# Kernel optimization log

Hardware: AMD Instinct MI355X
Metric: run time of the kernel (lower is better)

The kernel has to match this reference:

```python
import jax, jax.numpy as jnp
import numpy as np

DIM = 1024
N_HEADS = 16
HEAD_DIM = DIM // N_HEADS
MAX_SEQ_LEN = 2048
B, T = 2, 2048


def build_rope_cache(max_seq_len, head_dim):
    half_dim = head_dim // 2
    freq_seq = jnp.arange(half_dim, dtype=jnp.float32)
    inv_freq = 1.0 / 10000.0 ** (freq_seq / half_dim)
    t = jnp.arange(max_seq_len, dtype=jnp.float32)
    freqs = jnp.outer(t, inv_freq)                      # [S, half]
    emb = jnp.concatenate((freqs, freqs), axis=-1)      # [S, head_dim]
    cos = jnp.cos(emb)[None, :, None, :]                # [1, S, 1, head_dim]
    sin = jnp.sin(emb)[None, :, None, :]
    return cos, sin


def apply_rope(x, cos, sin):
    # x: [B, T, H, Dh]; cos/sin: [1, T, 1, Dh]
    x_even = x[..., ::2]
    x_odd = x[..., 1::2]
    cos_even = cos[..., ::2]
    sin_even = sin[..., ::2]
    x_even_rot = x_even * cos_even - x_odd * sin_even
    x_odd_rot = x_even * sin_even + x_odd * cos_even
    x_rot = jnp.stack([x_even_rot, x_odd_rot], axis=-1)  # [B,T,H,Dh/2,2]
    return x_rot.reshape(x.shape)


def setup_inputs() -> dict:
    key = jax.random.key(0)
    k1, k2, k3, k4, k5 = jax.random.split(key, 5)
    s = 0.02
    return {
        "x": jax.random.normal(k1, (B, T, DIM), dtype=jnp.float32),
        "attention_mask": jnp.ones((B, T), dtype=bool),
        "qkv_w": jax.random.normal(k2, (3 * DIM, DIM), dtype=jnp.float32) * s,
        "qkv_b": jax.random.normal(k3, (3 * DIM,), dtype=jnp.float32) * s,
        "out_w": jax.random.normal(k4, (DIM, DIM), dtype=jnp.float32) * s,
        "out_b": jax.random.normal(k5, (DIM,), dtype=jnp.float32) * s,
    }


def reference(x, attention_mask, qkv_w, qkv_b, out_w, out_b):
    Bx, Tx, _ = x.shape
    H, Dh = N_HEADS, HEAD_DIM
    scale = Dh ** (-0.5)

    qkv = x @ qkv_w.T + qkv_b                            # [B,T,3*dim]
    qkv = qkv.reshape(Bx, Tx, 3, H, Dh)
    q, k, v = qkv[:, :, 0], qkv[:, :, 1], qkv[:, :, 2]   # [B,T,H,Dh]

    cos, sin = build_rope_cache(MAX_SEQ_LEN, Dh)
    cos_all = cos[:, :Tx]
    sin_all = sin[:, :Tx]
    k = apply_rope(k, cos_all, sin_all)
    q = apply_rope(q, cos_all, sin_all)  # past_len = 0

    scores = jnp.einsum("bthd,bshd->bhts", q, k) * scale  # [B,H,T,S]

    causal = jnp.arange(Tx)[None, :] <= jnp.arange(Tx)[:, None]  # [T,S]
    scores = jnp.where(causal[None, None, :, :], scores, -jnp.inf)
    pad = attention_mask[:, None, None, :]                        # [B,1,1,S]
    scores = jnp.where(pad, scores, -jnp.inf)

    probs = jax.nn.softmax(scores, axis=-1)
    out = jnp.einsum("bhts,bshd->bthd", probs, v)        # [B,T,H,Dh]
    out = out.reshape(Bx, Tx, H * Dh)
    out = out @ out_w.T + out_b
    return out
```

## Files before the change

kernel.cpp:

```cpp
#include <hip/hip_runtime.h>
#include <stdint.h>

#define B_    2
#define T_    2048
#define DIM_  1024
#define NH_   16
#define DH_   64
#define MTOK  (B_*T_)

typedef __attribute__((ext_vector_type(8))) short bf16x8;
typedef __attribute__((ext_vector_type(4))) float f32x4;
typedef __attribute__((ext_vector_type(4))) short short4v;

__device__ __forceinline__ short f2bf(float f){
  union { float f; uint32_t u; } v; v.f = f;
  uint32_t u = v.u;
  return (short)((u + 0x7fffu + ((u>>16)&1u)) >> 16);
}

#define GLDS(g, l) __builtin_amdgcn_global_load_lds( \
    (const __attribute__((address_space(1))) void*)(g), \
    (__attribute__((address_space(3))) void*)(l), 16, 0, 0)

__global__ void convert_all(const float* __restrict__ x, const float* __restrict__ wq,
                            const float* __restrict__ wo,
                            short* __restrict__ xb, short* __restrict__ wqb,
                            short* __restrict__ wob, float* __restrict__ tbl){
  const int NX = MTOK*DIM_/4;
  const int NW = 3*DIM_*DIM_/4;
  const int NO = DIM_*DIM_/4;
  const int total = NX + NW + NO;
  const int gtid = blockIdx.x*blockDim.x + threadIdx.x;
  if (gtid < T_*32){
    int t = gtid >> 5, j = gtid & 31;
    float f = powf(10000.f, -(float)((2*j) & 31) / 32.f);
    float ang = (float)t * f;
    tbl[gtid*2]   = cosf(ang);
    tbl[gtid*2+1] = sinf(ang);
  }
  for (int i = gtid; i < total; i += gridDim.x*blockDim.x){
    const float* src; short* dst; int j;
    if (i < NX){ src = x;  dst = xb;  j = i; }
    else if (i < NX+NW){ src = wq; dst = wqb; j = i-NX; }
    else { src = wo; dst = wob; j = i-NX-NW; }
    float4 v = ((const float4*)src)[j];
    short4v o;
    o.x = f2bf(v.x); o.y = f2bf(v.y); o.z = f2bf(v.z); o.w = f2bf(v.w);
    ((short4v*)dst)[j] = o;
  }
}

template<int MODE>
__global__ __launch_bounds__(256,2)
void gemm_bt(const short* __restrict__ A, const short* __restrict__ Bw,
             const float* __restrict__ bias, float* __restrict__ outf,
             short* __restrict__ qb, short* __restrict__ kb, short* __restrict__ vb,
             const float* __restrict__ rtbl, int K, int N)
{
  __shared__ char smem[65536];
  const int tid  = threadIdx.x;
  const int wave = tid >> 6, lane = tid & 63;
  const int gx = gridDim.x;
  const int nwg = gx * gridDim.y;
  const int lid = blockIdx.x + blockIdx.y * gx;
  const int cpx = nwg >> 3;
  const int swz = (lid & 7) * cpx + (lid >> 3);
  const int bm = (swz / gx) << 7, bn = (swz % gx) << 7;
  const int wm = (wave >> 1) << 6, wn = (wave & 1) << 6;
  const int r16 = lane & 15, g4 = lane >> 4;
  const int slr = lane >> 3, slc = (lane & 7) << 4;

  f32x4 acc[4][4] = {};
  const int nt = K >> 6;

  auto stage = [&](int t, int buf){
    char* As = smem + (buf<<15);
    char* Bs = As + 16384;
    const int k0 = t << 6;
    #pragma unroll
    for (int sg = 0; sg < 4; ++sg){
      int row = (wave<<5) + (sg<<3) + slr;
      GLDS((const char*)A  + ((size_t)(bm+row)*K + k0)*2 + (slc ^ ((row&7)<<4)),
           As + ((wave<<5)+(sg<<3))*128);
      GLDS((const char*)Bw + ((size_t)(bn+row)*K + k0)*2 + (slc ^ ((row&7)<<4)),
           Bs + ((wave<<5)+(sg<<3))*128);
    }
  };

  stage(0, 0);
  asm volatile("s_waitcnt vmcnt(0)" ::: "memory");
  __syncthreads();

  for (int t = 0; t < nt; ++t){
    const int cur = t & 1;
    if (t + 1 < nt) stage(t+1, cur^1);
    char* As = smem + (cur<<15);
    char* Bs = As + 16384;
    #pragma unroll
    for (int ks = 0; ks < 2; ++ks){
      bf16x8 af[4], bfr[4];
      int bo = (ks<<6) + (g4<<4);
      #pragma unroll
      for (int mf = 0; mf < 4; ++mf){
        int row = wm + (mf<<4) + r16;
        af[mf] = *(const bf16x8*)(As + row*128 + (bo ^ ((row&7)<<4)));
      }
      #pragma unroll
      for (int nf = 0; nf < 4; ++nf){
        int row = wn + (nf<<4) + r16;
        bfr[nf] = *(const bf16x8*)(Bs + row*128 + (bo ^ ((row&7)<<4)));
      }
      __builtin_amdgcn_s_setprio(1);
      #pragma unroll
      for (int mf = 0; mf < 4; ++mf)
        #pragma unroll
        for (int nf = 0; nf < 4; ++nf)
          acc[mf][nf] = __builtin_amdgcn_mfma_f32_16x16x32_bf16(af[mf], bfr[nf], acc[mf][nf], 0, 0, 0);
      __builtin_amdgcn_s_setprio(0);
    }
    asm volatile("s_waitcnt vmcnt(0)" ::: "memory");
    __syncthreads();
  }

  if (MODE == 0){
    #pragma unroll
    for (int nf = 0; nf < 4; ++nf){
      int gn = bn + wn + (nf<<4) + r16;
      float bv = bias[gn];
      #pragma unroll
      for (int mf = 0; mf < 4; ++mf)
        #pragma unroll
        for (int j = 0; j < 4; ++j){
          int gm = bm + wm + (mf<<4) + (g4<<2) + j;
          outf[(size_t)gm*N + gn] = acc[mf][nf][j] + bv;
        }
    }
  } else {
    const int s = bn >> 10;
    if (s < 2){
      short* dst = s ? kb : qb;
      const float scq = s ? 1.0f : 0.125f;
      #pragma unroll
      for (int nf = 0; nf < 4; ++nf){
        int gn = bn + wn + (nf<<4) + r16;
        int d = gn & 63, h = (gn >> 6) & 15;
        int u = d >> 1;
        float sgn = (d & 1) ? 1.f : -1.f;
        float bv = bias[gn];
        #pragma unroll
        for (int mf = 0; mf < 4; ++mf){
          #pragma unroll
          for (int j = 0; j < 4; ++j){
            int gm = bm + wm + (mf<<4) + (g4<<2) + j;
            int b = gm >> 11, t = gm & (T_-1);
            float val = acc[mf][nf][j] + bv;
            float prt = __shfl_xor(val, 1);
            float2 cssn = ((const float2*)rtbl)[(t<<5) + u];
            float out = (val*cssn.x + prt*sgn*cssn.y) * scq;
            dst[(((size_t)(b*NH_+h))*T_ + t)*DH_ + d] = f2bf(out);
          }
        }
      }
    } else {
      #pragma unroll
      for (int nf = 0; nf < 4; ++nf){
        int gn = bn + wn + (nf<<4) + r16;
        int d = gn & 63, h = (gn >> 6) & 15;
        float bv = bias[gn];
        #pragma unroll
        for (int mf = 0; mf < 4; ++mf){
          int gm0 = bm + wm + (mf<<4) + (g4<<2);
          int b = gm0 >> 11, t0 = gm0 & (T_-1);
          short* vrow = vb + ((size_t)((b*NH_+h)*DH_ + d))*T_ + (t0 & ~63);
          int lo = t0 & 15, hi = (t0 & 63) >> 4;
          #pragma unroll
          for (int j = 0; j < 4; ++j)
            vrow[((lo + j) << 2) + hi] = f2bf(acc[mf][nf][j] + bv);
        }
      }
    }
  }
}

__global__ __launch_bounds__(256,2)
void attn_fwd(const short* __restrict__ q, const short* __restrict__ k,
              const short* __restrict__ vt, short* __restrict__ o)
{
  __shared__ char smem[40960];
  const int lid = blockIdx.x + (blockIdx.y << 4);
  const int swzid = (lid & 7) * 64 + (lid >> 3);
  const int p = swzid & 15, bh = swzid >> 4;
  const int qtA = 31 - p, qtB = p;
  const int tid = threadIdx.x, wave = tid >> 6, lane = tid & 63;
  char* Ps = smem + 32768 + wave*2048;
  const int r16 = lane & 15, g4 = lane >> 4;
  const int slr = lane >> 3, slc = (lane & 7) << 4;

  bf16x8 qfA[2], qfB[2];
  {
    size_t qrA = ((size_t)bh*T_ + (qtA<<6) + (wave<<4) + r16) * DH_;
    qfA[0] = *(const bf16x8*)(q + qrA + (g4<<3));
    qfA[1] = *(const bf16x8*)(q + qrA + 32 + (g4<<3));
    size_t qrB = ((size_t)bh*T_ + (qtB<<6) + (wave<<4) + r16) * DH_;
    qfB[0] = *(const bf16x8*)(q + qrB + (g4<<3));
    qfB[1] = *(const bf16x8*)(q + qrB + 32 + (g4<<3));
  }
  f32x4 oaccA[4] = {}, oaccB[4] = {};
  float rsA[4] = {0.f,0.f,0.f,0.f}, rsB[4] = {0.f,0.f,0.f,0.f};

  auto stage = [&](int c, int buf){
    char* Kb = smem + buf*8192;
    char* Vb = smem + 16384 + buf*8192;
    #pragma unroll
    for (int sg = 0; sg < 2; ++sg){
      int row = (wave<<4) + (sg<<3) + slr;
      const char* sk = (const char*)k  + (((size_t)bh*T_ + (c<<6) + row)*DH_)*2 + (slc ^ ((row&7)<<4));
      GLDS(sk, Kb + ((wave<<4)+(sg<<3))*128);
      const char* sv = (const char*)vt + (((size_t)bh*DH_ + row)*T_ + (c<<6))*2 + (slc ^ ((row&7)<<4));
      GLDS(sv, Vb + ((wave<<4)+(sg<<3))*128);
    }
  };

  stage(0, 0);
  asm volatile("s_waitcnt vmcnt(0)" ::: "memory");
  __syncthreads();

  for (int c = 0; c <= qtA; ++c){
    const int cur = c & 1;
    if (c < qtA) stage(c+1, cur^1);
    char* Kb = smem + cur*8192;
    char* Vb = smem + 16384 + cur*8192;

    #pragma unroll
    for (int tile = 0; tile < 2; ++tile){
      if (tile == 1 && c > qtB) break;
      const bf16x8* qf = tile ? qfB : qfA;
      f32x4* oacc = tile ? oaccB : oaccA;
      float* rs = tile ? rsB : rsA;
      const bool diag = (c == (tile ? qtB : qtA));

      f32x4 sc[4] = {};
      __builtin_amdgcn_s_setprio(1);
      #pragma unroll
      for (int ks = 0; ks < 2; ++ks){
        int bo = (ks<<6) + (g4<<4);
        #pragma unroll
        for (int nf = 0; nf < 4; ++nf){
          int row = (nf<<4) + r16;
          bf16x8 bk = *(const bf16x8*)(Kb + row*128 + (bo ^ ((row&7)<<4)));
          sc[nf] = __builtin_amdgcn_mfma_f32_16x16x32_bf16(qf[ks], bk, sc[nf], 0, 0, 0);
        }
      }
      __builtin_amdgcn_s_setprio(0);
      #pragma unroll
      for (int nf = 0; nf < 4; ++nf){
        #pragma unroll
        for (int j = 0; j < 4; ++j){
          float pv;
          if (diag){
            int colr = (nf<<4) + r16;
            int rowr = (wave<<4) + (g4<<2) + j;
            pv = (colr > rowr) ? 0.f : __expf(sc[nf][j]);
          } else {
            pv = __expf(sc[nf][j]);
          }
          sc[nf][j] = pv;
          rs[j] += pv;
        }
      }
      #pragma unroll
      for (int j = 0; j < 4; ++j){
        int prow = (g4<<2) + j;
        uint32_t lo, hi;
        asm("v_cvt_pk_bf16_f32 %0, %1, %2" : "=v"(lo) : "v"(sc[0][j]), "v"(sc[1][j]));
        asm("v_cvt_pk_bf16_f32 %0, %1, %2" : "=v"(hi) : "v"(sc[2][j]), "v"(sc[3][j]));
        uint2 pk; pk.x = lo; pk.y = hi;
        *(uint2*)(Ps + prow*128 + ((r16<<3) ^ ((prow&7)<<4))) = pk;
      }
      #pragma unroll
      for (int ks = 0; ks < 2; ++ks){
        int bo = (ks<<6) + (g4<<4);
        bf16x8 pa = *(const bf16x8*)(Ps + r16*128 + (bo ^ ((r16&7)<<4)));
        __builtin_amdgcn_s_setprio(1);
        #pragma unroll
        for (int nf = 0; nf < 4; ++nf){
          int row = (nf<<4) + r16;
          bf16x8 bv = *(const bf16x8*)(Vb + row*128 + (bo ^ ((row&7)<<4)));
          oacc[nf] = __builtin_amdgcn_mfma_f32_16x16x32_bf16(pa, bv, oacc[nf], 0, 0, 0);
        }
        __builtin_amdgcn_s_setprio(0);
      }
    }
    asm volatile("s_waitcnt vmcnt(0)" ::: "memory");
    __syncthreads();
  }

  const int b = bh >> 4, h = bh & 15;
  #pragma unroll
  for (int tile = 0; tile < 2; ++tile){
    const int qt = tile ? qtB : qtA;
    f32x4* oacc = tile ? oaccB : oaccA;
    float* rs = tile ? rsB : rsA;
    #pragma unroll
    for (int j = 0; j < 4; ++j){
      float s = rs[j];
      #pragma unroll
      for (int off = 1; off < 16; off <<= 1) s += __shfl_xor(s, off);
      float inv = 1.f / s;
      int t = (qt<<6) + (wave<<4) + (g4<<2) + j;
      #pragma unroll
      for (int nf = 0; nf < 4; ++nf){
        int d = (nf<<4) + r16;
        o[((size_t)(b*T_ + t))*DIM_ + h*DH_ + d] = f2bf(oacc[nf][j]*inv);
      }
    }
  }
}

extern "C" void kernel_launch(void* const* d_in, const int* in_sizes, int n_in,
                              void* d_out, int out_size, void* d_ws, size_t ws_size,
                              hipStream_t stream){
  const float* x     = (const float*)d_in[0];
  const float* qkv_w = (const float*)d_in[2];
  const float* qkv_b = (const float*)d_in[3];
  const float* out_w = (const float*)d_in[4];
  const float* out_b = (const float*)d_in[5];

  char* ws = (char*)d_ws;
  size_t off = 0;
  auto alloc = [&](size_t bytes){ void* p = ws + off; off += (bytes + 255) & ~(size_t)255; return p; };

  short* xb   = (short*)alloc((size_t)MTOK*DIM_*2);
  short* wqb  = (short*)alloc((size_t)3*DIM_*DIM_*2);
  short* wob  = (short*)alloc((size_t)DIM_*DIM_*2);
  short* qbuf = (short*)alloc((size_t)B_*NH_*T_*DH_*2);
  short* kbuf = (short*)alloc((size_t)B_*NH_*T_*DH_*2);
  short* vtr  = (short*)alloc((size_t)B_*NH_*DH_*T_*2);
  short* aout = (short*)alloc((size_t)MTOK*DIM_*2);
  float* tbl  = (float*)alloc((size_t)T_*32*2*4);

  convert_all<<<2048, 256, 0, stream>>>(x, qkv_w, out_w, xb, wqb, wob, tbl);
  gemm_bt<1><<<dim3(24,32), 256, 0, stream>>>(xb, wqb, qkv_b, nullptr,
                                              qbuf, kbuf, vtr, tbl, DIM_, 3*DIM_);
  attn_fwd<<<dim3(16,32), 256, 0, stream>>>(qbuf, kbuf, vtr, aout);
  gemm_bt<0><<<dim3(8,32), 256, 0, stream>>>(aout, wob, out_b, (float*)d_out,
                                             nullptr, nullptr, nullptr, tbl, DIM_, DIM_);
}
```

Measured before the change: 97.11 us.

## Replace QKV GEMM with 256x256-tile, 512-thread kernel using 4-stage LDS pipeline

The QKV projection gets its own kernel with 256x256 output tiles, 8 waves each computing 128x64, and a 4-slot ring of BK=32 LDS buffers with three stages in flight. Each stage is gated by vmcnt waits and a barrier. The larger tile is meant to cut global and LDS traffic per MFMA and to overlap loads with compute better. In exchange it launches only 192 workgroups at one per CU with 128KB of dynamic LDS, so fewer than the 256 CUs are used, and register pressure is higher. The output GEMM becomes a plain non-template kernel.

```diff
diff --git a/kernel.cpp b/kernel.cpp
--- a/kernel.cpp
+++ b/kernel.cpp
@@ -50,12 +50,126 @@
   }
 }
 
-template<int MODE>
+__global__ __launch_bounds__(512,1)
+void gemm256_qkv(const short* __restrict__ A, const short* __restrict__ Bw,
+                 const float* __restrict__ bias,
+                 short* __restrict__ qb, short* __restrict__ kb, short* __restrict__ vb,
+                 const float* __restrict__ rtbl)
+{
+  extern __shared__ char smem[];
+  const int K = 1024, nt = 32;
+  const int tid = threadIdx.x;
+  const int wave = tid >> 6, lane = tid & 63;
+  const int lid = blockIdx.x + blockIdx.y * 12;
+  const int swz = (lid & 7) * 24 + (lid >> 3);
+  const int bx = swz % 12, by = swz / 12;
+  const int bm = by << 8, bn = bx << 8;
+  const int wm = (wave >> 2) << 7;
+  const int wn = (wave & 3) << 6;
+  const int r16 = lane & 15, g4 = lane >> 4;
+  const int lrow = lane >> 2, lseg = lane & 3;
+
+  f32x4 acc[8][4] = {};
+
+  auto stage = [&](int t, int slot){
+    char* As = smem + (slot << 15);
+    char* Bs = As + 16384;
+    const int k0 = t << 5;
+    #pragma unroll
+    for (int i = 0; i < 2; ++i){
+      int row = (wave << 5) + (i << 4) + lrow;
+      int sseg = lseg ^ ((row >> 1) & 3);
+      GLDS((const char*)A  + ((size_t)(bm + row)*K + k0)*2 + (sseg << 4),
+           As + ((wave << 5) + (i << 4))*64);
+      GLDS((const char*)Bw + ((size_t)(bn + row)*K + k0)*2 + (sseg << 4),
+           Bs + ((wave << 5) + (i << 4))*64);
+    }
+  };
+
+  auto compute = [&](int slot){
+    char* As = smem + (slot << 15);
+    char* Bs = As + 16384;
+    bf16x8 af[8], bfr[4];
+    #pragma unroll
+    for (int mf = 0; mf < 8; ++mf){
+      int row = wm + (mf << 4) + r16;
+      af[mf] = *(const bf16x8*)(As + row*64 + (((g4 ^ (row >> 1)) & 3) << 4));
+    }
+    #pragma unroll
+    for (int nf = 0; nf < 4; ++nf){
+      int row = wn + (nf << 4) + r16;
+      bfr[nf] = *(const bf16x8*)(Bs + row*64 + (((g4 ^ (row >> 1)) & 3) << 4));
+    }
+    __builtin_amdgcn_s_setprio(1);
+    #pragma unroll
+    for (int mf = 0; mf < 8; ++mf)
+      #pragma unroll
+      for (int nf = 0; nf < 4; ++nf)
+        acc[mf][nf] = __builtin_amdgcn_mfma_f32_16x16x32_bf16(af[mf], bfr[nf], acc[mf][nf], 0, 0, 0);
+    __builtin_amdgcn_s_setprio(0);
+  };
+
+  stage(0, 0); stage(1, 1); stage(2, 2);
+
+  for (int t = 0; t < nt; ++t){
+    if (t < nt-2)       asm volatile("s_waitcnt vmcnt(8)" ::: "memory");
+    else if (t == nt-2) asm volatile("s_waitcnt vmcnt(4)" ::: "memory");
+    else                asm volatile("s_waitcnt vmcnt(0)" ::: "memory");
+    __builtin_amdgcn_s_barrier();
+    asm volatile("" ::: "memory");
+    if (t + 3 < nt) stage(t + 3, (t + 3) & 3);
+    compute(t & 3);
+  }
+
+  const int s = bn >> 10;
+  if (s < 2){
+    short* dst = s ? kb : qb;
+    const float scq = s ? 1.0f : 0.125f;
+    #pragma unroll
+    for (int nf = 0; nf < 4; ++nf){
+      int gn = bn + wn + (nf << 4) + r16;
+      int d = gn & 63, h = (gn >> 6) & 15;
+      int u = d >> 1;
+      float sgn = (d & 1) ? 1.f : -1.f;
+      float bv = bias[gn];
+      #pragma unroll
+      for (int mf = 0; mf < 8; ++mf){
+        #pragma unroll
+        for (int j = 0; j < 4; ++j){
+          int gm = bm + wm + (mf << 4) + (g4 << 2) + j;
+          int b = gm >> 11, t = gm & (T_-1);
+          float val = acc[mf][nf][j] + bv;
+          float prt = __shfl_xor(val, 1);
+          float2 cssn = ((const float2*)rtbl)[(t << 5) + u];
+          float out = (val*cssn.x + prt*sgn*cssn.y) * scq;
+          dst[(((size_t)(b*NH_+h))*T_ + t)*DH_ + d] = f2bf(out);
+        }
+      }
+    }
+  } else {
+    #pragma unroll
+    for (int nf = 0; nf < 4; ++nf){
+      int gn = bn + wn + (nf << 4) + r16;
+      int d = gn & 63, h = (gn >> 6) & 15;
+      float bv = bias[gn];
+      #pragma unroll
+      for (int mf = 0; mf < 8; ++mf){
+        int gm0 = bm + wm + (mf << 4) + (g4 << 2);
+        int b = gm0 >> 11, t0 = gm0 & (T_-1);
+        short* vrow = vb + ((size_t)((b*NH_+h)*DH_ + d))*T_ + (t0 & ~63);
+        int lo = t0 & 15, hi = (t0 & 63) >> 4;
+        #pragma unroll
+        for (int j = 0; j < 4; ++j)
+          vrow[((lo + j) << 2) + hi] = f2bf(acc[mf][nf][j] + bv);
+      }
+    }
+  }
+}
+
 __global__ __launch_bounds__(256,2)
-void gemm_bt(const short* __restrict__ A, const short* __restrict__ Bw,
-             const float* __restrict__ bias, float* __restrict__ outf,
-             short* __restrict__ qb, short* __restrict__ kb, short* __restrict__ vb,
-             const float* __restrict__ rtbl, int K, int N)
+void gemm_bt0(const short* __restrict__ A, const short* __restrict__ Bw,
+              const float* __restrict__ bias, float* __restrict__ outf,
+              int K, int N)
 {
   __shared__ char smem[65536];
   const int tid  = threadIdx.x;
@@ -122,63 +236,17 @@
     __syncthreads();
   }
 
-  if (MODE == 0){
-    #pragma unroll
-    for (int nf = 0; nf < 4; ++nf){
-      int gn = bn + wn + (nf<<4) + r16;
-      float bv = bias[gn];
-      #pragma unroll
-      for (int mf = 0; mf < 4; ++mf)
-        #pragma unroll
-        for (int j = 0; j < 4; ++j){
-          int gm = bm + wm + (mf<<4) + (g4<<2) + j;
-          outf[(size_t)gm*N + gn] = acc[mf][nf][j] + bv;
-        }
-    }
-  } else {
-    const int s = bn >> 10;
-    if (s < 2){
-      short* dst = s ? kb : qb;
-      const float scq = s ? 1.0f : 0.125f;
-      #pragma unroll
-      for (int nf = 0; nf < 4; ++nf){
-        int gn = bn + wn + (nf<<4) + r16;
-        int d = gn & 63, h = (gn >> 6) & 15;
-        int u = d >> 1;
-        float sgn = (d & 1) ? 1.f : -1.f;
-        float bv = bias[gn];
-        #pragma unroll
-        for (int mf = 0; mf < 4; ++mf){
-          #pragma unroll
-          for (int j = 0; j < 4; ++j){
-            int gm = bm + wm + (mf<<4) + (g4<<2) + j;
-            int b = gm >> 11, t = gm & (T_-1);
-            float val = acc[mf][nf][j] + bv;
-            float prt = __shfl_xor(val, 1);
-            float2 cssn = ((const float2*)rtbl)[(t<<5) + u];
-            float out = (val*cssn.x + prt*sgn*cssn.y) * scq;
-            dst[(((size_t)(b*NH_+h))*T_ + t)*DH_ + d] = f2bf(out);
-          }
-        }
-      }
-    } else {
-      #pragma unroll
-      for (int nf = 0; nf < 4; ++nf){
-        int gn = bn + wn + (nf<<4) + r16;
-        int d = gn & 63, h = (gn >> 6) & 15;
-        float bv = bias[gn];
-        #pragma unroll
-        for (int mf = 0; mf < 4; ++mf){
-          int gm0 = bm + wm + (mf<<4) + (g4<<2);
-          int b = gm0 >> 11, t0 = gm0 & (T_-1);
-          short* vrow = vb + ((size_t)((b*NH_+h)*DH_ + d))*T_ + (t0 & ~63);
-          int lo = t0 & 15, hi = (t0 & 63) >> 4;
-          #pragma unroll
-          for (int j = 0; j < 4; ++j)
-            vrow[((lo + j) << 2) + hi] = f2bf(acc[mf][nf][j] + bv);
-        }
-      }
-    }
+  #pragma unroll
+  for (int nf = 0; nf < 4; ++nf){
+    int gn = bn + wn + (nf<<4) + r16;
+    float bv = bias[gn];
+    #pragma unroll
+    for (int mf = 0; mf < 4; ++mf)
+      #pragma unroll
+      for (int j = 0; j < 4; ++j){
+        int gm = bm + wm + (mf<<4) + (g4<<2) + j;
+        outf[(size_t)gm*N + gn] = acc[mf][nf][j] + bv;
+      }
   }
 }
 
@@ -340,9 +408,9 @@
   float* tbl  = (float*)alloc((size_t)T_*32*2*4);
 
   convert_all<<<2048, 256, 0, stream>>>(x, qkv_w, out_w, xb, wqb, wob, tbl);
-  gemm_bt<1><<<dim3(24,32), 256, 0, stream>>>(xb, wqb, qkv_b, nullptr,
-                                              qbuf, kbuf, vtr, tbl, DIM_, 3*DIM_);
+  gemm256_qkv<<<dim3(12,16), 512, 131072, stream>>>(xb, wqb, qkv_b,
+                                                    qbuf, kbuf, vtr, tbl);
   attn_fwd<<<dim3(16,32), 256, 0, stream>>>(qbuf, kbuf, vtr, aout);
-  gemm_bt<0><<<dim3(8,32), 256, 0, stream>>>(aout, wob, out_b, (float*)d_out,
-                                             nullptr, nullptr, nullptr, tbl, DIM_, DIM_);
-}
+  gemm_bt0<<<dim3(8,32), 256, 0, stream>>>(aout, wob, out_b, (float*)d_out,
+                                           DIM_, DIM_);
+}
```

Result: no change. 97.10 us (-0.0%).
